# Kernel optimization log

Hardware: AMD Instinct MI355X
Metric: run time of the kernel (lower is better)

The kernel has to match this reference:

```python
import jax, jax.numpy as jnp
import numpy as np

B, T, N, H, F, E = 8, 64, 2048, 64, 64, 32768
G = 3 * H  # GRU gate dim


def setup_inputs() -> dict:
    key = jax.random.key(0)
    ks = jax.random.split(key, 12)
    s = 0.05
    return {
        "x": jax.random.normal(ks[0], (B, T, N, F), jnp.float32),
        "targets": jax.random.normal(ks[1], (B, T, N, 1), jnp.float32),
        "targets_mask": jax.random.uniform(ks[2], (B, T, N, 1)) > 0.2,
        "edge_index": jax.random.randint(ks[3], (2, E), 0, N),
        "W_msg": jax.random.normal(ks[4], (H, H), jnp.float32) * s,
        "b_msg": jnp.zeros((H,), jnp.float32),
        "W_mix": jax.random.normal(ks[5], (H, H + F), jnp.float32) * s,
        "b_mix": jnp.zeros((H,), jnp.float32),
        "W_ih": jax.random.normal(ks[6], (N, G, H), jnp.float32) * s,
        "W_hh": jax.random.normal(ks[7], (N, G, H), jnp.float32) * s,
        "b_ih": jnp.zeros((N, G), jnp.float32),
        "b_hh": jnp.zeros((N, G), jnp.float32),
        "W_read": jax.random.normal(ks[8], (1, H), jnp.float32) * s,
        "b_read": jnp.zeros((1,), jnp.float32),
    }


def reference(x, targets, targets_mask, edge_index,
              W_msg, b_msg, W_mix, b_mix,
              W_ih, W_hh, b_ih, b_hh, W_read, b_read):
    src, dst = edge_index[0], edge_index[1]

    def step(state, x_t):
        # state: [B,N,H], x_t: [B,N,F]
        m = jnp.einsum('bnh,gh->bng', state, W_msg) + b_msg           # state_to_message
        agg = jnp.zeros_like(m).at[:, dst, :].add(m[:, src, :])       # add-aggregate over directed edges
        mi = jnp.concatenate([agg, x_t], axis=-1)                     # [B,N,H+F]
        m2 = jnp.einsum('bnf,hf->bnh', mi, W_mix) + b_mix             # mix_input
        # per-node independent GRU cells (batched weights [N,3H,*])
        gi = jnp.einsum('bnh,ngh->bng', m2, W_ih) + b_ih
        gh = jnp.einsum('bnh,ngh->bng', state, W_hh) + b_hh
        i_r, i_z, i_n = jnp.split(gi, 3, axis=-1)
        h_r, h_z, h_n = jnp.split(gh, 3, axis=-1)
        r = jax.nn.sigmoid(i_r + h_r)
        z = jax.nn.sigmoid(i_z + h_z)
        n_cand = jnp.tanh(i_n + r * h_n)
        new_state = (1.0 - z) * n_cand + z * state
        out = jnp.einsum('bnh,oh->bno', new_state, W_read) + b_read   # readout -> [B,N,1]
        return new_state, out

    state0 = jnp.zeros((B, N, H), x.dtype)
    _, outs = jax.lax.scan(step, state0, jnp.swapaxes(x, 0, 1))       # outs: [T,B,N,1]
    outputs = jnp.swapaxes(outs, 0, 1)                                # [B,T,N,1]
    loss = 0.5 * (outputs - targets) ** 2
    mask = targets_mask.astype(loss.dtype)
    return jnp.sum(loss * mask) / jnp.sum(mask)                       # masked mean
```

## Files before the change

kernel.cpp:

```cpp
#include <hip/hip_runtime.h>
#include <math.h>

namespace {
constexpr int B = 8, T = 64, N = 2048, H = 64, F = 64, E = 32768, G = 192;
constexpr int BNH = B * N * H;
constexpr int NWELEM = N * G * H;
constexpr int NBLK = 1024;
}

typedef __attribute__((ext_vector_type(8))) short bfrag;
typedef __attribute__((ext_vector_type(4))) float ffrag;
typedef long f8frag;

#define MFMA(a, b, c)  __builtin_amdgcn_mfma_f32_16x16x32_bf16(a, b, c, 0, 0, 0)
#define MFMA8(a, b, c) __builtin_amdgcn_mfma_f32_16x16x32_fp8_fp8(a, b, c, 0, 0, 0)

#define DS (1.f / 512.f)

__device__ __forceinline__ unsigned short f2bf(float f) {
  unsigned u = __float_as_uint(f);
  u += 0x7fffu + ((u >> 16) & 1u);
  return (unsigned short)(u >> 16);
}
__device__ __forceinline__ float bf2f(unsigned short u) {
  return __uint_as_float(((unsigned)u) << 16);
}
template<bool HI>
__device__ __forceinline__ unsigned cvtpk8(float a, float b, unsigned old) {
  return __builtin_amdgcn_cvt_pk_fp8_f32(a, b, old, HI);
}

__device__ __forceinline__ void grid_bar(int* bar, int t) {
  __syncthreads();
  if (threadIdx.x == 0) {
    __hip_atomic_fetch_add(&bar[(blockIdx.x & 63) * 16], 1,
                           __ATOMIC_RELAXED, __HIP_MEMORY_SCOPE_AGENT);
  }
  if (blockIdx.x == 0) {
    if (threadIdx.x < 64) {
      while (__hip_atomic_load(&bar[threadIdx.x * 16],
                               __ATOMIC_RELAXED, __HIP_MEMORY_SCOPE_AGENT) < 16 * (t + 1))
        __builtin_amdgcn_s_sleep(1);
      if (threadIdx.x == 0)
        __hip_atomic_store(&bar[4096], t + 1, __ATOMIC_RELAXED, __HIP_MEMORY_SCOPE_AGENT);
    }
  } else if (threadIdx.x == 0) {
    while (__hip_atomic_load(&bar[4096], __ATOMIC_RELAXED, __HIP_MEMORY_SCOPE_AGENT) < t + 1)
      __builtin_amdgcn_s_sleep(2);
  }
  asm volatile("" ::: "memory");
  __syncthreads();
}


__global__ __launch_bounds__(256) void init_kernel(
    unsigned short* __restrict__ buf0, const float* __restrict__ b_msg,
    float* __restrict__ loss_acc, float* __restrict__ scal,
    int* __restrict__ deg, int* __restrict__ bar)
{
  int stride = gridDim.x * blockDim.x;
  for (int i = blockIdx.x * blockDim.x + threadIdx.x; i < BNH; i += stride) {
    buf0[i] = f2bf(b_msg[i & (H - 1)]);
    if (i < 8192) bar[i] = 0;
    if (i < N) { loss_acc[i] = 0.f; deg[i] = 0; }
    if (i < 16) scal[i] = 0.f;
  }
}

__global__ __launch_bounds__(256) void conv_kernel(
    const float* __restrict__ Wi, const float* __restrict__ Wh,
    const float* __restrict__ Wm, const float* __restrict__ Wg,
    unsigned char* __restrict__ Wib, unsigned char* __restrict__ Whb,
    unsigned short* __restrict__ Wmb, unsigned short* __restrict__ Wgb)
{
  int stride = gridDim.x * blockDim.x * 2;
  for (int i = (blockIdx.x * blockDim.x + threadIdx.x) * 2; i < NWELEM; i += stride) {
    unsigned p = cvtpk8<false>(Wi[i] * 32.f, Wi[i + 1] * 32.f, 0u);
    *(unsigned short*)(Wib + i) = (unsigned short)p;
    p = cvtpk8<false>(Wh[i] * 32.f, Wh[i + 1] * 32.f, 0u);
    *(unsigned short*)(Whb + i) = (unsigned short)p;
    if (i < 64 * 128) { Wmb[i] = f2bf(Wm[i]); Wmb[i + 1] = f2bf(Wm[i + 1]); }
    if (i < 64 * 64)  { Wgb[i] = f2bf(Wg[i]); Wgb[i + 1] = f2bf(Wg[i + 1]); }
  }
}

__global__ __launch_bounds__(256) void hist_kernel(const int* __restrict__ ei, int* __restrict__ deg) {
  int e = blockIdx.x * 256 + threadIdx.x;
  if (e < E) atomicAdd(&deg[ei[E + e]], 1);
}

__global__ __launch_bounds__(1024) void scan_kernel(const int* __restrict__ deg,
    int* __restrict__ row_ptr, int* __restrict__ cursor)
{
  __shared__ int s[N];
  int tid = threadIdx.x;
  s[tid] = deg[tid];
  s[tid + 1024] = deg[tid + 1024];
  __syncthreads();
  for (int off = 1; off < N; off <<= 1) {
    int v0 = (tid >= off) ? s[tid - off] : 0;
    int v1 = s[tid + 1024 - off];
    __syncthreads();
    s[tid] += v0;
    s[tid + 1024] += v1;
    __syncthreads();
  }
  row_ptr[tid + 1] = s[tid];
  row_ptr[tid + 1025] = s[tid + 1024];
  cursor[tid] = (tid == 0) ? 0 : s[tid - 1];
  cursor[tid + 1024] = s[tid + 1023];
  if (tid == 0) row_ptr[0] = 0;
}

__global__ __launch_bounds__(256) void fill_kernel(const int* __restrict__ ei,
    int* __restrict__ cursor, int* __restrict__ col_src)
{
  int e = blockIdx.x * 256 + threadIdx.x;
  if (e < E) {
    int d = ei[E + e];
    int slot = atomicAdd(&cursor[d], 1);
    col_src[slot] = ei[e];
  }
}

__global__ __launch_bounds__(256) void mask_kernel(const int* __restrict__ mask, float* __restrict__ scal) {
  int stride = gridDim.x * blockDim.x;
  int v = 0;
  for (int i = blockIdx.x * blockDim.x + threadIdx.x; i < B * T * N; i += stride)
    v += (mask[i] != 0);
  for (int o = 1; o < 64; o <<= 1) v += __shfl_xor(v, o, 64);
  if ((threadIdx.x & 63) == 0) atomicAdd(&scal[0], (float)v);
}


__global__ __attribute__((amdgpu_flat_work_group_size(256, 256), amdgpu_waves_per_eu(4, 4)))
void persist_kernel(
    const float* __restrict__ x, const float* __restrict__ targets,
    const int* __restrict__ mask,
    const unsigned char* __restrict__ W_ihb, const unsigned char* __restrict__ W_hhb,
    const unsigned short* __restrict__ W_mixb, const unsigned short* __restrict__ W_msgb,
    const float* __restrict__ b_ih, const float* __restrict__ b_hh,
    const float* __restrict__ b_mix, const float* __restrict__ b_msg,
    const float* __restrict__ W_read, const float* __restrict__ b_read,
    const int* __restrict__ row_ptr, const int* __restrict__ col_src,
    unsigned short* bufs,
    float* __restrict__ loss_acc, int* __restrict__ bar)
{
  __shared__ float sts[2][8][64];
  __shared__ float partial[4][8][72];
  __shared__ unsigned char m2F8[8 * 80];
  __shared__ unsigned short nsA[8 * 72];
  __shared__ float redS[4][8];

  const int tid = threadIdx.x;
  const int w = tid >> 6, lane = tid & 63;
  const int mrow = lane & 15, quad = lane >> 4;
  const int n0 = blockIdx.x * 2;
  const bfrag za = (bfrag)0;
  const int hcol = w * 16 + mrow;

  f8frag whf[2][6], wif[2][6];
#pragma unroll
  for (int k = 0; k < 2; ++k) {
    const unsigned char* Wh = W_hhb + (size_t)(n0 + k) * (G * H);
    const unsigned char* Wi = W_ihb + (size_t)(n0 + k) * (G * H);
#pragma unroll
    for (int tt = 0; tt < 3; ++tt) {
      const int off = ((w + tt * 4) * 16 + mrow) * H + quad * 8;
      whf[k][2 * tt]     = *(const f8frag*)(Wh + off);
      whf[k][2 * tt + 1] = *(const f8frag*)(Wh + off + 32);
      wif[k][2 * tt]     = *(const f8frag*)(Wi + off);
      wif[k][2 * tt + 1] = *(const f8frag*)(Wi + off + 32);
    }
  }
  const unsigned short* wmp = W_mixb + hcol * 128 + quad * 8;
  const unsigned short* wgp = W_msgb + hcol * H + quad * 8;

  float bir[2], biz[2], bin_[2], bhr[2], bhz[2], bhn[2];
#pragma unroll
  for (int k = 0; k < 2; ++k) {
    const int bg = (n0 + k) * G + hcol;
    bir[k] = b_ih[bg]; biz[k] = b_ih[bg + 64]; bin_[k] = b_ih[bg + 128];
    bhr[k] = b_hh[bg]; bhz[k] = b_hh[bg + 64]; bhn[k] = b_hh[bg + 128];
  }
  float wrd = W_read[hcol];
  float bmix = b_mix[hcol];
  float bmsg = b_msg[hcol];
  const float brd = b_read[0];
  const int e0a = row_ptr[n0], e0b = row_ptr[n0 + 1], e0c = row_ptr[n0 + 2];

#pragma unroll
  for (int k = 0; k < 2; ++k) {
#pragma unroll
    for (int j = 0; j < 6; ++j) {
      asm volatile("" : "+v"(whf[k][j]));
      asm volatile("" : "+v"(wif[k][j]));
    }
    asm volatile("" : "+v"(bir[k]), "+v"(biz[k]), "+v"(bin_[k]),
                      "+v"(bhr[k]), "+v"(bhz[k]), "+v"(bhn[k]));
  }
  asm volatile("" : "+v"(wrd), "+v"(bmix), "+v"(bmsg));

  for (int i = tid; i < 2 * 8 * 64; i += 256) ((float*)sts)[i] = 0.f;
  __syncthreads();

  float lsum[2] = {0.f, 0.f};
  const unsigned short* mcur = bufs;
  unsigned short* mnxt = bufs + BNH;

#pragma unroll 1
  for (int t = 0; t < T; ++t) {
#pragma unroll
    for (int k = 0; k < 2; ++k) {
      const int nn = n0 + k;
      const int ee0 = k ? e0b : e0a;
      const int ee1 = k ? e0c : e0b;

      f8frag asF0 = 0, asF1 = 0;
      bfrag a2 = za, a3 = za;
      if (mrow < 8) {
        const float* sp = &sts[k][mrow][0];
        {
          float4 s0 = *(const float4*)(sp + quad * 8);
          float4 s1 = *(const float4*)(sp + quad * 8 + 4);
          unsigned u0 = 0, u1 = 0;
          u0 = cvtpk8<false>(s0.x * 16.f, s0.y * 16.f, u0);
          u0 = cvtpk8<true >(s0.z * 16.f, s0.w * 16.f, u0);
          u1 = cvtpk8<false>(s1.x * 16.f, s1.y * 16.f, u1);
          u1 = cvtpk8<true >(s1.z * 16.f, s1.w * 16.f, u1);
          asF0 = (f8frag)(((unsigned long long)u1 << 32) | u0);
          s0 = *(const float4*)(sp + 32 + quad * 8);
          s1 = *(const float4*)(sp + 32 + quad * 8 + 4);
          u0 = 0; u1 = 0;
          u0 = cvtpk8<false>(s0.x * 16.f, s0.y * 16.f, u0);
          u0 = cvtpk8<true >(s0.z * 16.f, s0.w * 16.f, u0);
          u1 = cvtpk8<false>(s1.x * 16.f, s1.y * 16.f, u1);
          u1 = cvtpk8<true >(s1.z * 16.f, s1.w * 16.f, u1);
          asF1 = (f8frag)(((unsigned long long)u1 << 32) | u0);
        }
        const float* xp = x + (((size_t)mrow * T + t) * N + nn) * F;
        {
          float4 t0 = *(const float4*)(xp + quad * 8);
          float4 t1 = *(const float4*)(xp + quad * 8 + 4);
          a2[0]=(short)f2bf(t0.x); a2[1]=(short)f2bf(t0.y); a2[2]=(short)f2bf(t0.z); a2[3]=(short)f2bf(t0.w);
          a2[4]=(short)f2bf(t1.x); a2[5]=(short)f2bf(t1.y); a2[6]=(short)f2bf(t1.z); a2[7]=(short)f2bf(t1.w);
          t0 = *(const float4*)(xp + 32 + quad * 8);
          t1 = *(const float4*)(xp + 32 + quad * 8 + 4);
          a3[0]=(short)f2bf(t0.x); a3[1]=(short)f2bf(t0.y); a3[2]=(short)f2bf(t0.z); a3[3]=(short)f2bf(t0.w);
          a3[4]=(short)f2bf(t1.x); a3[5]=(short)f2bf(t1.y); a3[6]=(short)f2bf(t1.z); a3[7]=(short)f2bf(t1.w);
        }
      }
      {
        float accL[4] = {0.f,0.f,0.f,0.f}, accH[4] = {0.f,0.f,0.f,0.f};
        const int j = lane & 31, bh = lane >> 5;
        const unsigned* mcU = (const unsigned*)mcur;
        for (int e = ee0 + w; e < ee1; e += 4) {
          const unsigned* mp = mcU + (size_t)col_src[e] * 256 + bh * 32 + j;
#pragma unroll
          for (int bb = 0; bb < 4; ++bb) {
            unsigned v = mp[bb * 64];
            accL[bb] += bf2f((unsigned short)(v & 0xffffu));
            accH[bb] += bf2f((unsigned short)(v >> 16));
          }
        }
#pragma unroll
        for (int bb = 0; bb < 4; ++bb) {
          partial[w][bb * 2 + bh][2 * j]     = accL[bb];
          partial[w][bb * 2 + bh][2 * j + 1] = accH[bb];
        }
      }
      ffrag ah0 = {0.f,0.f,0.f,0.f}, ah1 = {0.f,0.f,0.f,0.f}, ah2 = {0.f,0.f,0.f,0.f};
      ah0 = MFMA8(asF0, whf[k][0], ah0); ah0 = MFMA8(asF1, whf[k][1], ah0);
      ah1 = MFMA8(asF0, whf[k][2], ah1); ah1 = MFMA8(asF1, whf[k][3], ah1);
      ah2 = MFMA8(asF0, whf[k][4], ah2); ah2 = MFMA8(asF1, whf[k][5], ah2);
      __syncthreads();

      {
        bfrag wm0 = *(const bfrag*)(wmp);
        bfrag wm1 = *(const bfrag*)(wmp + 32);
        bfrag wm2 = *(const bfrag*)(wmp + 64);
        bfrag wm3 = *(const bfrag*)(wmp + 96);
        bfrag a0 = za, a1 = za;
        if (mrow < 8) {
          const float* p = &partial[0][mrow][quad * 8];
#pragma unroll
          for (int j = 0; j < 8; ++j) {
            float s = p[j] + p[j + 576] + p[j + 1152] + p[j + 1728];
            a0[j] = (short)f2bf(s);
          }
          const float* p2 = &partial[0][mrow][32 + quad * 8];
#pragma unroll
          for (int j = 0; j < 8; ++j) {
            float s = p2[j] + p2[j + 576] + p2[j + 1152] + p2[j + 1728];
            a1[j] = (short)f2bf(s);
          }
        }
        ffrag accm = {0.f, 0.f, 0.f, 0.f};
        accm = MFMA(a0, wm0, accm);
        accm = MFMA(a1, wm1, accm);
        accm = MFMA(a2, wm2, accm);
        accm = MFMA(a3, wm3, accm);
        if (quad < 2) {
#pragma unroll
          for (int r = 0; r < 4; ++r) {
            unsigned p = cvtpk8<false>((accm[r] + bmix) * 16.f, 0.f, 0u);
            m2F8[(quad * 4 + r) * 80 + hcol] = (unsigned char)(p & 0xffu);
          }
        }
      }
      __syncthreads();

      {
        f8frag amF0 = 0, amF1 = 0;
        if (mrow < 8) {
          amF0 = *(const f8frag*)&m2F8[mrow * 80 + quad * 8];
          amF1 = *(const f8frag*)&m2F8[mrow * 80 + 32 + quad * 8];
        }
        ffrag ai0 = {0.f,0.f,0.f,0.f}, ai1 = {0.f,0.f,0.f,0.f}, ai2 = {0.f,0.f,0.f,0.f};
        ai0 = MFMA8(amF0, wif[k][0], ai0); ai0 = MFMA8(amF1, wif[k][1], ai0);
        ai1 = MFMA8(amF0, wif[k][2], ai1); ai1 = MFMA8(amF1, wif[k][3], ai1);
        ai2 = MFMA8(amF0, wif[k][4], ai2); ai2 = MFMA8(amF1, wif[k][5], ai2);
        if (quad < 2) {
          float v[4];
#pragma unroll
          for (int r = 0; r < 4; ++r) {
            const int b = quad * 4 + r;
            float rs  = (ai0[r] + ah0[r]) * DS + bir[k] + bhr[k];
            float zs  = (ai1[r] + ah1[r]) * DS + biz[k] + bhz[k];
            float in_ = ai2[r] * DS + bin_[k];
            float hn  = ah2[r] * DS + bhn[k];
            float rg = 1.f / (1.f + __expf(-rs));
            float z  = 1.f / (1.f + __expf(-zs));
            float pre = in_ + rg * hn;
            float a = __expf(-2.f * fabsf(pre));
            float nc = copysignf((1.f - a) / (1.f + a), pre);
            float sold = sts[k][b][hcol];
            float ns = (1.f - z) * nc + z * sold;
            sts[k][b][hcol] = ns;
            nsA[b * 72 + hcol] = f2bf(ns);
            v[r] = ns * wrd;
          }
#pragma unroll
          for (int o = 1; o < 16; o <<= 1) {
#pragma unroll
            for (int r = 0; r < 4; ++r) v[r] += __shfl_xor(v[r], o, 64);
          }
          if (mrow == 0) {
#pragma unroll
            for (int r = 0; r < 4; ++r) redS[w][quad * 4 + r] = v[r];
          }
        }
      }
      __syncthreads();

      {
        bfrag wg0 = *(const bfrag*)(wgp);
        bfrag wg1 = *(const bfrag*)(wgp + 32);
        bfrag an0 = za, an1 = za;
        if (mrow < 8) {
          an0 = *(const bfrag*)&nsA[mrow * 72 + quad * 8];
          an1 = *(const bfrag*)&nsA[mrow * 72 + 32 + quad * 8];
        }
        ffrag accg = {0.f, 0.f, 0.f, 0.f};
        accg = MFMA(an0, wg0, accg);
        accg = MFMA(an1, wg1, accg);
        if (quad < 2) {
          unsigned* mnU = (unsigned*)mnxt;
          const int jcol = hcol >> 1;
#pragma unroll
          for (int r = 0; r < 4; ++r) {
            float v0 = accg[r] + bmsg;
            float v1 = __shfl_xor(v0, 1, 64);
            if (!(mrow & 1)) {
              unsigned pk = (unsigned)f2bf(v0) | ((unsigned)f2bf(v1) << 16);
              __hip_atomic_store(&mnU[(size_t)nn * 256 + (quad * 4 + r) * 32 + jcol],
                                 pk, __ATOMIC_RELAXED, __HIP_MEMORY_SCOPE_AGENT);
            }
          }
        }
      }
      if (tid < 8) {
        float vv = redS[0][tid] + redS[1][tid] + redS[2][tid] + redS[3][tid] + brd;
        size_t idx = ((size_t)tid * T + t) * N + nn;
        float d = vv - targets[idx];
        float l = (mask[idx] != 0) ? 0.5f * d * d : 0.f;
        l += __shfl_xor(l, 1, 64);
        l += __shfl_xor(l, 2, 64);
        l += __shfl_xor(l, 4, 64);
        if (tid == 0) lsum[k] += l;
      }
    }
    grid_bar(bar, t);
    mcur = mnxt;
    mnxt += BNH;
  }
  if (tid == 0) { loss_acc[n0] = lsum[0]; loss_acc[n0 + 1] = lsum[1]; }
}

__global__ __launch_bounds__(256) void final_kernel(const float* __restrict__ loss_acc,
    const float* __restrict__ scal, float* __restrict__ out)
{
  __shared__ float sred[4];
  float v = 0.f;
  for (int i = threadIdx.x; i < N; i += 256) v += loss_acc[i];
  for (int o = 1; o < 64; o <<= 1) v += __shfl_xor(v, o, 64);
  if ((threadIdx.x & 63) == 0) sred[threadIdx.x >> 6] = v;
  __syncthreads();
  if (threadIdx.x == 0) out[0] = (sred[0] + sred[1] + sred[2] + sred[3]) / scal[0];
}

extern "C" void kernel_launch(void* const* d_in, const int* in_sizes, int n_in,
                              void* d_out, int out_size, void* d_ws, size_t ws_size,
                              hipStream_t stream)
{
  const float* x       = (const float*)d_in[0];
  const float* targets = (const float*)d_in[1];
  const int*   mask    = (const int*)d_in[2];
  const int*   ei      = (const int*)d_in[3];
  const float* W_msg   = (const float*)d_in[4];
  const float* b_msg   = (const float*)d_in[5];
  const float* W_mix   = (const float*)d_in[6];
  const float* b_mix   = (const float*)d_in[7];
  const float* W_ih    = (const float*)d_in[8];
  const float* W_hh    = (const float*)d_in[9];
  const float* b_ih    = (const float*)d_in[10];
  const float* b_hh    = (const float*)d_in[11];
  const float* W_read  = (const float*)d_in[12];
  const float* b_read  = (const float*)d_in[13];
  float* out = (float*)d_out;

  unsigned short* bufs  = (unsigned short*)d_ws;
  float* loss_acc       = (float*)(bufs + (size_t)(T + 1) * BNH);
  float* scal           = loss_acc + N;
  int* deg              = (int*)(scal + 16);
  int* row_ptr          = deg + N;
  int* cursor           = row_ptr + (N + 16);
  int* col_src          = cursor + N;
  int* bar              = col_src + E;
  unsigned char* W_ihb  = (unsigned char*)(bar + 8192);
  unsigned char* W_hhb  = W_ihb + NWELEM;
  unsigned short* W_mixb = (unsigned short*)(W_hhb + NWELEM);
  unsigned short* W_msgb = W_mixb + 64 * 128;

  init_kernel<<<1024, 256, 0, stream>>>(bufs, b_msg, loss_acc, scal, deg, bar);
  conv_kernel<<<8192, 256, 0, stream>>>(W_ih, W_hh, W_mix, W_msg, W_ihb, W_hhb, W_mixb, W_msgb);
  hist_kernel<<<E / 256, 256, 0, stream>>>(ei, deg);
  scan_kernel<<<1, 1024, 0, stream>>>(deg, row_ptr, cursor);
  fill_kernel<<<E / 256, 256, 0, stream>>>(ei, cursor, col_src);
  mask_kernel<<<512, 256, 0, stream>>>(mask, scal);

  persist_kernel<<<NBLK, 256, 0, stream>>>(x, targets, mask,
                                           W_ihb, W_hhb, W_mixb, W_msgb,
                                           b_ih, b_hh, b_mix, b_msg, W_read, b_read,
                                           row_ptr, col_src, bufs, loss_acc, bar);

  final_kernel<<<1, 256, 0, stream>>>(loss_acc, scal, out);
}
```

Before: 2.186 ms.

## Replace global grid barrier with per-block dataflow flags over graph neighbors

```diff
diff --git a/kernel.cpp b/kernel.cpp
--- a/kernel.cpp
+++ b/kernel.cpp
@@ -6,6 +6,7 @@
 constexpr int BNH = B * N * H;
 constexpr int NWELEM = N * G * H;
 constexpr int NBLK = 1024;
+constexpr int SLMAX = 192;
 }
 
 typedef __attribute__((ext_vector_type(8))) short bfrag;
@@ -28,28 +29,6 @@
 template<bool HI>
 __device__ __forceinline__ unsigned cvtpk8(float a, float b, unsigned old) {
   return __builtin_amdgcn_cvt_pk_fp8_f32(a, b, old, HI);
-}
-
-__device__ __forceinline__ void grid_bar(int* bar, int t) {
-  __syncthreads();
-  if (threadIdx.x == 0) {
-    __hip_atomic_fetch_add(&bar[(blockIdx.x & 63) * 16], 1,
-                           __ATOMIC_RELAXED, __HIP_MEMORY_SCOPE_AGENT);
-  }
-  if (blockIdx.x == 0) {
-    if (threadIdx.x < 64) {
-      while (__hip_atomic_load(&bar[threadIdx.x * 16],
-                               __ATOMIC_RELAXED, __HIP_MEMORY_SCOPE_AGENT) < 16 * (t + 1))
-        __builtin_amdgcn_s_sleep(1);
-      if (threadIdx.x == 0)
-        __hip_atomic_store(&bar[4096], t + 1, __ATOMIC_RELAXED, __HIP_MEMORY_SCOPE_AGENT);
-    }
-  } else if (threadIdx.x == 0) {
-    while (__hip_atomic_load(&bar[4096], __ATOMIC_RELAXED, __HIP_MEMORY_SCOPE_AGENT) < t + 1)
-      __builtin_amdgcn_s_sleep(2);
-  }
-  asm volatile("" ::: "memory");
-  __syncthreads();
 }
 
 
@@ -123,6 +102,26 @@
   }
 }
 
+__global__ __launch_bounds__(256) void dep_kernel(const int* __restrict__ row_ptr,
+    const int* __restrict__ col_src, int* __restrict__ slist, int* __restrict__ scnt)
+{
+  int b = blockIdx.x * 256 + threadIdx.x;
+  if (b >= NBLK) return;
+  const int e0 = row_ptr[2 * b], e1 = row_ptr[2 * b + 2];
+  int* out = slist + (size_t)b * SLMAX;
+  int cnt = 0;
+  for (int e = e0; e < e1; ++e) {
+    int sb = col_src[e] >> 1;
+    bool dup = false;
+    for (int i = 0; i < cnt; ++i) if (out[i] == sb) { dup = true; break; }
+    if (!dup) {
+      if (cnt < SLMAX) out[cnt++] = sb;
+      else { cnt = -1; break; }
+    }
+  }
+  scnt[b] = cnt;
+}
+
 __global__ __launch_bounds__(256) void mask_kernel(const int* __restrict__ mask, float* __restrict__ scal) {
   int stride = gridDim.x * blockDim.x;
   int v = 0;
@@ -144,13 +143,16 @@
     const float* __restrict__ W_read, const float* __restrict__ b_read,
     const int* __restrict__ row_ptr, const int* __restrict__ col_src,
     unsigned short* bufs,
-    float* __restrict__ loss_acc, int* __restrict__ bar)
+    float* __restrict__ loss_acc, int* __restrict__ bar,
+    const int* __restrict__ slist, const int* __restrict__ scnt)
 {
   __shared__ float sts[2][8][64];
   __shared__ float partial[4][8][72];
   __shared__ unsigned char m2F8[8 * 80];
   __shared__ unsigned short nsA[8 * 72];
   __shared__ float redS[4][8];
+  __shared__ int sl[SLMAX];
+  __shared__ int slc;
 
   const int tid = threadIdx.x;
   const int w = tid >> 6, lane = tid & 63;
@@ -202,6 +204,11 @@
   asm volatile("" : "+v"(wrd), "+v"(bmix), "+v"(bmsg));
 
   for (int i = tid; i < 2 * 8 * 64; i += 256) ((float*)sts)[i] = 0.f;
+  {
+    const int* slg = slist + (size_t)blockIdx.x * SLMAX;
+    for (int i = tid; i < SLMAX; i += 256) sl[i] = slg[i];
+    if (tid == 0) slc = scnt[blockIdx.x];
+  }
   __syncthreads();
 
   float lsum[2] = {0.f, 0.f};
@@ -210,6 +217,27 @@
 
 #pragma unroll 1
   for (int t = 0; t < T; ++t) {
+    if (t > 0) {
+      if (tid < 64) {
+        const int cnt = slc;
+        if (cnt >= 0) {
+          for (int i = tid; i < cnt; i += 64) {
+            const int sb = sl[i];
+            while (__hip_atomic_load(&bar[sb * 8], __ATOMIC_RELAXED,
+                                     __HIP_MEMORY_SCOPE_AGENT) < t)
+              __builtin_amdgcn_s_sleep(1);
+          }
+        } else {
+          for (int i = tid; i < NBLK; i += 64) {
+            while (__hip_atomic_load(&bar[i * 8], __ATOMIC_RELAXED,
+                                     __HIP_MEMORY_SCOPE_AGENT) < t)
+              __builtin_amdgcn_s_sleep(1);
+          }
+        }
+      }
+      asm volatile("" ::: "memory");
+      __syncthreads();
+    }
 #pragma unroll
     for (int k = 0; k < 2; ++k) {
       const int nn = n0 + k;
@@ -390,7 +418,10 @@
         if (tid == 0) lsum[k] += l;
       }
     }
-    grid_bar(bar, t);
+    __syncthreads();
+    if (tid == 0)
+      __hip_atomic_store(&bar[blockIdx.x * 8], t + 1,
+                         __ATOMIC_RELAXED, __HIP_MEMORY_SCOPE_AGENT);
     mcur = mnxt;
     mnxt += BNH;
   }
@@ -437,7 +468,9 @@
   int* cursor           = row_ptr + (N + 16);
   int* col_src          = cursor + N;
   int* bar              = col_src + E;
-  unsigned char* W_ihb  = (unsigned char*)(bar + 8192);
+  int* slist            = bar + 8192;
+  int* scnt             = slist + NBLK * SLMAX;
+  unsigned char* W_ihb  = (unsigned char*)(scnt + NBLK);
   unsigned char* W_hhb  = W_ihb + NWELEM;
   unsigned short* W_mixb = (unsigned short*)(W_hhb + NWELEM);
   unsigned short* W_msgb = W_mixb + 64 * 128;
@@ -447,12 +480,14 @@
   hist_kernel<<<E / 256, 256, 0, stream>>>(ei, deg);
   scan_kernel<<<1, 1024, 0, stream>>>(deg, row_ptr, cursor);
   fill_kernel<<<E / 256, 256, 0, stream>>>(ei, cursor, col_src);
+  dep_kernel<<<4, 256, 0, stream>>>(row_ptr, col_src, slist, scnt);
   mask_kernel<<<512, 256, 0, stream>>>(mask, scal);
 
   persist_kernel<<<NBLK, 256, 0, stream>>>(x, targets, mask,
                                            W_ihb, W_hhb, W_mixb, W_msgb,
                                            b_ih, b_hh, b_mix, b_msg, W_read, b_read,
-                                           row_ptr, col_src, bufs, loss_acc, bar);
+                                           row_ptr, col_src, bufs, loss_acc, bar,
+                                           slist, scnt);
 
   final_kernel<<<1, 256, 0, stream>>>(loss_acc, scal, out);
 }
```

New measurement: 2.620 ms. +19.9%, slower.
